# Kernel optimization log

Measured on AMD Instinct MI355X. Metric: run time of the kernel, lower is better.

## Reference

```python
import jax, jax.numpy as jnp
import numpy as np

N, K, D = 524288, 32, 8
EPS = 1e-6


def setup_inputs() -> dict:
    key = jax.random.key(0)
    k1, k2, k3, k4 = jax.random.split(key, 4)
    x = jax.random.normal(k1, (N, D), dtype=jnp.float32)
    pi = jax.random.uniform(k2, (K,), dtype=jnp.float32)
    means = jax.random.normal(k3, (K, D), dtype=jnp.float32)
    # eye + small perturbation keeps tril(chol_var) well-conditioned (PD covariance)
    chol_var = jnp.eye(D, dtype=jnp.float32)[None] + 0.1 * jax.random.normal(k4, (K, D, D), dtype=jnp.float32)
    return {"x": x, "pi": pi, "means": means, "chol_var": chol_var}


def reference(x, pi, means, chol_var):
    d = x.shape[-1]
    L = jnp.tril(chol_var)                                   # [K,d,d]
    cov = jnp.einsum('kij,klj->kil', L, L) + EPS * jnp.eye(d, dtype=x.dtype)
    C = jnp.linalg.cholesky(cov)                             # [K,d,d] (MVN recomputes cholesky)
    logdet = 2.0 * jnp.sum(jnp.log(jnp.diagonal(C, axis1=-2, axis2=-1)), axis=-1)  # [K]
    eye = jnp.eye(d, dtype=x.dtype)
    Cinv = jax.vmap(lambda c: jax.scipy.linalg.solve_triangular(c, eye, lower=True))(C)  # [K,d,d]
    zx = jnp.einsum('kij,nj->nki', Cinv, x)                  # [N,K,d]
    zm = jnp.einsum('kij,kj->ki', Cinv, means)               # [K,d]
    maha = jnp.sum((zx - zm[None]) ** 2, axis=-1)            # [N,K]
    log_2pi = jnp.log(2.0 * jnp.pi).astype(x.dtype)
    log_probs = -0.5 * (maha + d * log_2pi + logdet[None])   # [N,K]
    wll = log_probs + jax.nn.log_softmax(pi)[None]
    return jax.scipy.special.logsumexp(wll, axis=1)          # [N]
```

## Files before the change

kernel.cpp:

```cpp
#include <hip/hip_runtime.h>
#include <math.h>

#define K_ 32
#define D_ 8
#define NF 48
#define NTHREADS 256
#define NBLOCKS 1024
#define TPW 4

typedef _Float16 half8 __attribute__((ext_vector_type(8)));
typedef float f32x16 __attribute__((ext_vector_type(16)));

__global__ __launch_bounds__(NTHREADS) void gmm_mfma(
    const float* __restrict__ x,
    const float* __restrict__ pi,
    const float* __restrict__ means,
    const float* __restrict__ chol,
    float* __restrict__ out, int N)
{
    __shared__ __align__(16) _Float16 ldsA[3][64][8];

    const int tid = threadIdx.x;

    if (tid < K_) {
        const int k = tid;
        float L[D_][D_];
#pragma unroll
        for (int i = 0; i < D_; ++i)
#pragma unroll
            for (int j = 0; j <= i; ++j)
                L[i][j] = chol[k * 64 + i * 8 + j];

        float rd[D_];
#pragma unroll
        for (int i = 0; i < D_; ++i) rd[i] = 1.f / L[i][i];

        float Ci[D_][D_];
#pragma unroll
        for (int j = 0; j < D_; ++j) {
            Ci[j][j] = rd[j];
#pragma unroll
            for (int i = j + 1; i < D_; ++i) {
                float s = 0.f;
#pragma unroll
                for (int m = j; m < i; ++m) s += L[i][m] * Ci[m][j];
                Ci[i][j] = -s * rd[i];
            }
        }

        float logdet = 0.f;
#pragma unroll
        for (int i = 0; i < D_; ++i) logdet += __logf(fabsf(L[i][i]));
        logdet *= 2.f;

        float A2[D_][D_];
#pragma unroll
        for (int i = 0; i < D_; ++i)
#pragma unroll
            for (int j = 0; j <= i; ++j) {
                float s = 0.f;
#pragma unroll
                for (int m = i; m < D_; ++m) s += Ci[m][i] * Ci[m][j];
                A2[i][j] = s;
                A2[j][i] = s;
            }

        float mu[D_];
#pragma unroll
        for (int j = 0; j < D_; ++j) mu[j] = means[k * 8 + j];
        float b[D_], q = 0.f;
#pragma unroll
        for (int i = 0; i < D_; ++i) {
            float s = 0.f;
#pragma unroll
            for (int j = 0; j < D_; ++j) s += A2[i][j] * mu[j];
            b[i] = s;
            q += s * mu[i];
        }

        float mx = pi[0];
#pragma unroll
        for (int t = 1; t < K_; ++t) mx = fmaxf(mx, pi[t]);
        float se = 0.f;
#pragma unroll
        for (int t = 0; t < K_; ++t) se += __expf(pi[t] - mx);
        float lse = mx + __logf(se);

        const float LOG2PI = 1.8378770664093453f;
        const float LOG2E  = 1.4426950408889634f;
        const float ALPHA  = 0.72134752044448170f;
        float cst2 = ((pi[k] - lse) - 0.5f * (logdet + 8.f * LOG2PI)) * LOG2E;

        float V[NF];
        int t = 0;
#pragma unroll
        for (int i = 0; i < D_; ++i)
#pragma unroll
            for (int j = 0; j <= i; ++j)
                V[t++] = (i == j) ? -ALPHA * A2[i][i] : -2.f * ALPHA * A2[i][j];
#pragma unroll
        for (int i = 0; i < D_; ++i) V[36 + i] = 2.f * ALPHA * b[i];
        V[44] = cst2 - ALPHA * q;
        V[45] = 0.f; V[46] = 0.f; V[47] = 0.f;

#pragma unroll
        for (int s = 0; s < 3; ++s)
#pragma unroll
            for (int h = 0; h < 2; ++h)
#pragma unroll
                for (int j = 0; j < 8; ++j)
                    ldsA[s][h * 32 + k][j] = (_Float16)V[16 * s + 8 * h + j];
    }
    __syncthreads();

    const int lane = tid & 63;
    const int m    = lane & 31;
    const bool h1  = lane >= 32;

    half8 wf[3];
#pragma unroll
    for (int s = 0; s < 3; ++s) wf[s] = *(const half8*)&ldsA[s][lane][0];

    const int w  = blockIdx.x * (NTHREADS / 64) + (tid >> 6);
    const int t0 = w * TPW;
    const float4* xp = (const float4*)x;
    const float LN2 = 0.69314718055994531f;

    float xv[TPW][D_];
#pragma unroll
    for (int u = 0; u < TPW; ++u) {
        const int n = (t0 + u) * 32 + m;
        float4 a = xp[2 * n], b2 = xp[2 * n + 1];
        xv[u][0] = a.x;  xv[u][1] = a.y;  xv[u][2] = a.z;  xv[u][3] = a.w;
        xv[u][4] = b2.x; xv[u][5] = b2.y; xv[u][6] = b2.z; xv[u][7] = b2.w;
    }

#pragma unroll
    for (int u = 0; u < TPW; ++u) {
        float Y[NF];
        {
            int t = 0;
#pragma unroll
            for (int i = 0; i < D_; ++i)
#pragma unroll
                for (int j = 0; j <= i; ++j) Y[t++] = xv[u][i] * xv[u][j];
#pragma unroll
            for (int i = 0; i < D_; ++i) Y[36 + i] = xv[u][i];
            Y[44] = 1.f; Y[45] = 0.f; Y[46] = 0.f; Y[47] = 0.f;
        }

        f32x16 acc;
#pragma unroll
        for (int r = 0; r < 16; ++r) acc[r] = 0.f;

#pragma unroll
        for (int s = 0; s < 3; ++s) {
            half8 bf;
#pragma unroll
            for (int j = 0; j < 8; ++j) {
                float v = h1 ? Y[16 * s + 8 + j] : Y[16 * s + j];
                bf[j] = (_Float16)v;
            }
            acc = __builtin_amdgcn_mfma_f32_32x32x16_f16(wf[s], bf, acc, 0, 0, 0);
        }

        float tot = 0.f;
#pragma unroll
        for (int r = 0; r < 16; ++r) tot += exp2f(acc[r]);
        tot += __shfl_xor(tot, 32, 64);
        float res = log2f(tot) * LN2;
        if (!h1) out[(t0 + u) * 32 + m] = res;
    }
}

extern "C" void kernel_launch(void* const* d_in, const int* in_sizes, int n_in,
                              void* d_out, int out_size, void* d_ws, size_t ws_size,
                              hipStream_t stream) {
    const float* x     = (const float*)d_in[0];
    const float* pi    = (const float*)d_in[1];
    const float* means = (const float*)d_in[2];
    const float* chol  = (const float*)d_in[3];
    float* out = (float*)d_out;

    int N = in_sizes[0] / D_;

    gmm_mfma<<<NBLOCKS, NTHREADS, 0, stream>>>(x, pi, means, chol, out, N);
}
```

Baseline: 74.34 us.

## Hoist per-component precompute into a separate single-block kernel via workspace

```diff
diff --git a/kernel.cpp b/kernel.cpp
--- a/kernel.cpp
+++ b/kernel.cpp
@@ -5,121 +5,120 @@
 #define D_ 8
 #define NF 48
 #define NTHREADS 256
-#define NBLOCKS 1024
-#define TPW 4
+#define TPW 2
+#define NBLOCKS 2048
 
 typedef _Float16 half8 __attribute__((ext_vector_type(8)));
 typedef float f32x16 __attribute__((ext_vector_type(16)));
 
+__global__ void gmm_precompute(const float* __restrict__ pi,
+                               const float* __restrict__ means,
+                               const float* __restrict__ chol,
+                               _Float16* __restrict__ wsA) {
+    const int l = threadIdx.x;
+    const int k = l & 31;
+
+    float L[D_][D_];
+#pragma unroll
+    for (int i = 0; i < D_; ++i)
+#pragma unroll
+        for (int j = 0; j <= i; ++j)
+            L[i][j] = chol[k * 64 + i * 8 + j];
+
+    float rd[D_];
+#pragma unroll
+    for (int i = 0; i < D_; ++i) rd[i] = 1.f / L[i][i];
+
+    float Ci[D_][D_];
+#pragma unroll
+    for (int j = 0; j < D_; ++j) {
+        Ci[j][j] = rd[j];
+#pragma unroll
+        for (int i = j + 1; i < D_; ++i) {
+            float s = 0.f;
+#pragma unroll
+            for (int m = j; m < i; ++m) s += L[i][m] * Ci[m][j];
+            Ci[i][j] = -s * rd[i];
+        }
+    }
+
+    float logdet = 0.f;
+#pragma unroll
+    for (int i = 0; i < D_; ++i) logdet += __logf(fabsf(L[i][i]));
+    logdet *= 2.f;
+
+    float A2[D_][D_];
+#pragma unroll
+    for (int i = 0; i < D_; ++i)
+#pragma unroll
+        for (int j = 0; j <= i; ++j) {
+            float s = 0.f;
+#pragma unroll
+            for (int m = i; m < D_; ++m) s += Ci[m][i] * Ci[m][j];
+            A2[i][j] = s;
+            A2[j][i] = s;
+        }
+
+    float mu[D_];
+#pragma unroll
+    for (int j = 0; j < D_; ++j) mu[j] = means[k * 8 + j];
+    float b[D_], q = 0.f;
+#pragma unroll
+    for (int i = 0; i < D_; ++i) {
+        float s = 0.f;
+#pragma unroll
+        for (int j = 0; j < D_; ++j) s += A2[i][j] * mu[j];
+        b[i] = s;
+        q += s * mu[i];
+    }
+
+    float mx = pi[0];
+#pragma unroll
+    for (int t = 1; t < K_; ++t) mx = fmaxf(mx, pi[t]);
+    float se = 0.f;
+#pragma unroll
+    for (int t = 0; t < K_; ++t) se += __expf(pi[t] - mx);
+    float lse = mx + __logf(se);
+
+    const float LOG2PI = 1.8378770664093453f;
+    const float LOG2E  = 1.4426950408889634f;
+    const float ALPHA  = 0.72134752044448170f;
+    float cst2 = ((pi[k] - lse) - 0.5f * (logdet + 8.f * LOG2PI)) * LOG2E;
+
+    float V[NF];
+    int t = 0;
+#pragma unroll
+    for (int i = 0; i < D_; ++i)
+#pragma unroll
+        for (int j = 0; j <= i; ++j)
+            V[t++] = (i == j) ? -ALPHA * A2[i][i] : -2.f * ALPHA * A2[i][j];
+#pragma unroll
+    for (int i = 0; i < D_; ++i) V[36 + i] = 2.f * ALPHA * b[i];
+    V[44] = cst2 - ALPHA * q;
+    V[45] = 0.f; V[46] = 0.f; V[47] = 0.f;
+
+    const int h = l >> 5;
+#pragma unroll
+    for (int s = 0; s < 3; ++s)
+#pragma unroll
+        for (int j = 0; j < 8; ++j)
+            wsA[s * 512 + l * 8 + j] = (_Float16)V[16 * s + 8 * h + j];
+}
+
 __global__ __launch_bounds__(NTHREADS) void gmm_mfma(
     const float* __restrict__ x,
-    const float* __restrict__ pi,
-    const float* __restrict__ means,
-    const float* __restrict__ chol,
+    const _Float16* __restrict__ wsA,
     float* __restrict__ out, int N)
 {
-    __shared__ __align__(16) _Float16 ldsA[3][64][8];
-
-    const int tid = threadIdx.x;
-
-    if (tid < K_) {
-        const int k = tid;
-        float L[D_][D_];
-#pragma unroll
-        for (int i = 0; i < D_; ++i)
-#pragma unroll
-            for (int j = 0; j <= i; ++j)
-                L[i][j] = chol[k * 64 + i * 8 + j];
-
-        float rd[D_];
-#pragma unroll
-        for (int i = 0; i < D_; ++i) rd[i] = 1.f / L[i][i];
-
-        float Ci[D_][D_];
-#pragma unroll
-        for (int j = 0; j < D_; ++j) {
-            Ci[j][j] = rd[j];
-#pragma unroll
-            for (int i = j + 1; i < D_; ++i) {
-                float s = 0.f;
-#pragma unroll
-                for (int m = j; m < i; ++m) s += L[i][m] * Ci[m][j];
-                Ci[i][j] = -s * rd[i];
-            }
-        }
-
-        float logdet = 0.f;
-#pragma unroll
-        for (int i = 0; i < D_; ++i) logdet += __logf(fabsf(L[i][i]));
-        logdet *= 2.f;
-
-        float A2[D_][D_];
-#pragma unroll
-        for (int i = 0; i < D_; ++i)
-#pragma unroll
-            for (int j = 0; j <= i; ++j) {
-                float s = 0.f;
-#pragma unroll
-                for (int m = i; m < D_; ++m) s += Ci[m][i] * Ci[m][j];
-                A2[i][j] = s;
-                A2[j][i] = s;
-            }
-
-        float mu[D_];
-#pragma unroll
-        for (int j = 0; j < D_; ++j) mu[j] = means[k * 8 + j];
-        float b[D_], q = 0.f;
-#pragma unroll
-        for (int i = 0; i < D_; ++i) {
-            float s = 0.f;
-#pragma unroll
-            for (int j = 0; j < D_; ++j) s += A2[i][j] * mu[j];
-            b[i] = s;
-            q += s * mu[i];
-        }
-
-        float mx = pi[0];
-#pragma unroll
-        for (int t = 1; t < K_; ++t) mx = fmaxf(mx, pi[t]);
-        float se = 0.f;
-#pragma unroll
-        for (int t = 0; t < K_; ++t) se += __expf(pi[t] - mx);
-        float lse = mx + __logf(se);
-
-        const float LOG2PI = 1.8378770664093453f;
-        const float LOG2E  = 1.4426950408889634f;
-        const float ALPHA  = 0.72134752044448170f;
-        float cst2 = ((pi[k] - lse) - 0.5f * (logdet + 8.f * LOG2PI)) * LOG2E;
-
-        float V[NF];
-        int t = 0;
-#pragma unroll
-        for (int i = 0; i < D_; ++i)
-#pragma unroll
-            for (int j = 0; j <= i; ++j)
-                V[t++] = (i == j) ? -ALPHA * A2[i][i] : -2.f * ALPHA * A2[i][j];
-#pragma unroll
-        for (int i = 0; i < D_; ++i) V[36 + i] = 2.f * ALPHA * b[i];
-        V[44] = cst2 - ALPHA * q;
-        V[45] = 0.f; V[46] = 0.f; V[47] = 0.f;
-
-#pragma unroll
-        for (int s = 0; s < 3; ++s)
-#pragma unroll
-            for (int h = 0; h < 2; ++h)
-#pragma unroll
-                for (int j = 0; j < 8; ++j)
-                    ldsA[s][h * 32 + k][j] = (_Float16)V[16 * s + 8 * h + j];
-    }
-    __syncthreads();
-
+    const int tid  = threadIdx.x;
     const int lane = tid & 63;
     const int m    = lane & 31;
-    const bool h1  = lane >= 32;
+    const int h    = lane >> 5;
 
     half8 wf[3];
 #pragma unroll
-    for (int s = 0; s < 3; ++s) wf[s] = *(const half8*)&ldsA[s][lane][0];
+    for (int s = 0; s < 3; ++s)
+        wf[s] = *(const half8*)(wsA + s * 512 + lane * 8);
 
     const int w  = blockIdx.x * (NTHREADS / 64) + (tid >> 6);
     const int t0 = w * TPW;
@@ -137,18 +136,6 @@
 
 #pragma unroll
     for (int u = 0; u < TPW; ++u) {
-        float Y[NF];
-        {
-            int t = 0;
-#pragma unroll
-            for (int i = 0; i < D_; ++i)
-#pragma unroll
-                for (int j = 0; j <= i; ++j) Y[t++] = xv[u][i] * xv[u][j];
-#pragma unroll
-            for (int i = 0; i < D_; ++i) Y[36 + i] = xv[u][i];
-            Y[44] = 1.f; Y[45] = 0.f; Y[46] = 0.f; Y[47] = 0.f;
-        }
-
         f32x16 acc;
 #pragma unroll
         for (int r = 0; r < 16; ++r) acc[r] = 0.f;
@@ -158,7 +145,20 @@
             half8 bf;
 #pragma unroll
             for (int j = 0; j < 8; ++j) {
-                float v = h1 ? Y[16 * s + 8 + j] : Y[16 * s + j];
+                const int f = 16 * s + 8 * h + j;
+                float v;
+                if (f < 36) {
+                    int fi = 0;
+                    while ((fi + 1) * (fi + 2) / 2 <= f) ++fi;
+                    int fj = f - fi * (fi + 1) / 2;
+                    v = xv[u][fi] * xv[u][fj];
+                } else if (f < 44) {
+                    v = xv[u][f - 36];
+                } else if (f == 44) {
+                    v = 1.f;
+                } else {
+                    v = 0.f;
+                }
                 bf[j] = (_Float16)v;
             }
             acc = __builtin_amdgcn_mfma_f32_32x32x16_f16(wf[s], bf, acc, 0, 0, 0);
@@ -169,7 +169,7 @@
         for (int r = 0; r < 16; ++r) tot += exp2f(acc[r]);
         tot += __shfl_xor(tot, 32, 64);
         float res = log2f(tot) * LN2;
-        if (!h1) out[(t0 + u) * 32 + m] = res;
+        if (h == 0) out[(t0 + u) * 32 + m] = res;
     }
 }
 
@@ -181,8 +181,10 @@
     const float* means = (const float*)d_in[2];
     const float* chol  = (const float*)d_in[3];
     float* out = (float*)d_out;
+    _Float16* wsA = (_Float16*)d_ws;
 
     int N = in_sizes[0] / D_;
 
-    gmm_mfma<<<NBLOCKS, NTHREADS, 0, stream>>>(x, pi, means, chol, out, N);
+    gmm_precompute<<<1, 64, 0, stream>>>(pi, means, chol, wsA);
+    gmm_mfma<<<NBLOCKS, NTHREADS, 0, stream>>>(x, wsA, out, N);
 }
```

New measurement: 123.3 us. 1.66x slower.
